# Performance work log

Hardware: AMD Instinct MI355X
Metric: run time of the kernel (lower is better)

The kernel has to match this reference:

```python
import jax, jax.numpy as jnp
import numpy as np

DIM = 768
NUM_HEADS = 12
HEAD_DIM = DIM // NUM_HEADS
SCALE = HEAD_DIM ** -0.5
NEG = -9e15


def setup_inputs() -> dict:
    key = jax.random.key(0)
    ks = jax.random.split(key, 8)
    B, N, M, C = 4, 1024, 2048, DIM
    q = jax.random.normal(ks[0], (B, N, C), dtype=jnp.float32)
    kv = jax.random.normal(ks[1], (B, M, C), dtype=jnp.float32)
    mask = jax.random.randint(ks[2], (B, 1, N, M), 0, 2, dtype=jnp.int32)
    s = 1.0 / np.sqrt(C)
    Wq = jax.random.normal(ks[3], (C, C), dtype=jnp.float32) * s      # nn.Linear(dim, dim), no bias
    Wkv = jax.random.normal(ks[4], (2 * C, C), dtype=jnp.float32) * s  # nn.Linear(dim, 2*dim), no bias
    Wproj = jax.random.normal(ks[5], (C, C), dtype=jnp.float32) * s
    bproj = jax.random.normal(ks[6], (C,), dtype=jnp.float32) * s
    return {"q": q, "kv": kv, "Wq": Wq, "Wkv": Wkv, "Wproj": Wproj, "bproj": bproj, "mask": mask}


def reference(q, kv, Wq, Wkv, Wproj, bproj, mask):
    B, M, C = kv.shape
    _, N, _ = q.shape
    H, d = NUM_HEADS, HEAD_DIM
    # kv projection -> [B, M, 2, H, d] -> k, v: [B, H, M, d]
    kvp = (kv @ Wkv.T).reshape(B, M, 2, H, d)
    k = kvp[:, :, 0].transpose(0, 2, 1, 3)
    v = kvp[:, :, 1].transpose(0, 2, 1, 3)
    # q projection -> [B, H, N, d], pre-scaled
    qp = (q @ Wq.T).reshape(B, N, H, d).transpose(0, 2, 1, 3) * SCALE
    attn = jnp.einsum('bhnd,bhmd->bhnm', qp, k)  # [B, H, N, M]
    attn = jnp.where(mask == 0, NEG, attn)
    attn = jax.nn.softmax(attn, axis=-1)
    # attn_drop / proj_drop have rate 0.0 (eval): identity
    x = jnp.einsum('bhnm,bhmd->bhnd', attn, v)
    x = x.transpose(0, 2, 1, 3).reshape(B, N, C)
    x = x @ Wproj.T + bproj
    return x
```

## Files before the change

### kernel.cpp

```cpp
#include <hip/hip_runtime.h>
#include <hip/hip_bf16.h>


typedef short    s16x8  __attribute__((ext_vector_type(8)));
typedef short    s16x4  __attribute__((ext_vector_type(4)));
typedef float    f32x4  __attribute__((ext_vector_type(4)));
typedef _Float16 f16x8  __attribute__((ext_vector_type(8)));
typedef _Float16 f16x4  __attribute__((ext_vector_type(4)));
typedef _Float16 f16x2  __attribute__((ext_vector_type(2)));

#define NUM_H 12
#define DIM   768
#define NQ    1024
#define MK    2048
#define QK_SCALE_LOG2E 0.18033688f

__device__ __forceinline__ short f2h(float v) {
    _Float16 h = (_Float16)v;
    return __builtin_bit_cast(short, h);
}
__device__ __forceinline__ f32x4 mfma16x32(f16x8 a, f16x8 b, f32x4 c) {
    return __builtin_amdgcn_mfma_f32_16x16x32_f16(a, b, c, 0, 0, 0);
}
__device__ __forceinline__ f16x2 pk2h(float a, float b) {
    return __builtin_bit_cast(f16x2, __builtin_amdgcn_cvt_pkrtz(a, b));
}
__device__ __forceinline__ void gl_lds16(const short* g, short* l) {
    __builtin_amdgcn_global_load_lds(
        (const __attribute__((address_space(1))) unsigned int*)g,
        (__attribute__((address_space(3))) unsigned int*)l, 16, 0, 0);
}

__global__ __launch_bounds__(256) void prep_kernel(
    const float* __restrict__ q, const float* __restrict__ kv,
    const float* __restrict__ Wq, const float* __restrict__ Wkv,
    const float* __restrict__ Wp, const int* __restrict__ mask,
    short* __restrict__ q_h, short* __restrict__ kv_h,
    short* __restrict__ Wq_h, short* __restrict__ Wkv_h,
    short* __restrict__ Wp_h, unsigned char* __restrict__ mbytes)
{
    int bid = blockIdx.x;
    if (bid < 5760) {
        const float* s; short* d; long base;
        if (bid < 1536)      { s = q;   d = q_h;   base = (long)bid * 2048; }
        else if (bid < 4608) { s = kv;  d = kv_h;  base = (long)(bid - 1536) * 2048; }
        else if (bid < 4896) { s = Wq;  d = Wq_h;  base = (long)(bid - 4608) * 2048; }
        else if (bid < 5472) { s = Wkv; d = Wkv_h; base = (long)(bid - 4896) * 2048; }
        else                 { s = Wp;  d = Wp_h;  base = (long)(bid - 5472) * 2048; }
        long i = base + threadIdx.x * 8;
        float4 a = *(const float4*)(s + i);
        float4 b = *(const float4*)(s + i + 4);
        s16x8 r;
        r[0] = f2h(a.x); r[1] = f2h(a.y); r[2] = f2h(a.z); r[3] = f2h(a.w);
        r[4] = f2h(b.x); r[5] = f2h(b.y); r[6] = f2h(b.z); r[7] = f2h(b.w);
        *(s16x8*)(d + i) = r;
    } else {
        long base = (long)(bid - 5760) * 2048 + threadIdx.x * 8;
        int4 m0 = *(const int4*)(mask + base);
        int4 m1 = *(const int4*)(mask + base + 4);
        unsigned v = (unsigned)(m0.x != 0)        | ((unsigned)(m0.y != 0) << 1)
                   | ((unsigned)(m0.z != 0) << 2) | ((unsigned)(m0.w != 0) << 3)
                   | ((unsigned)(m1.x != 0) << 4) | ((unsigned)(m1.y != 0) << 5)
                   | ((unsigned)(m1.z != 0) << 6) | ((unsigned)(m1.w != 0) << 7);
        mbytes[base >> 3] = (unsigned char)v;
    }
}

__device__ __forceinline__ void gemm_core(
    short* smem,
    const short* __restrict__ A, const short* __restrict__ Bt,
    int Ncols, int mode, const float* __restrict__ bias,
    short* __restrict__ outb, short* __restrict__ outb2,
    float* __restrict__ outf, int bid)
{
    short (*As)[64] = (short(*)[64])smem;
    short (*Bs)[64] = (short(*)[64])(smem + 8192);

    int ntiles = Ncols >> 7;
    int m0 = (bid / ntiles) << 7;
    int n0 = (bid % ntiles) << 7;
    int t = threadIdx.x;
    int w = t >> 6, lane = t & 63, quad = lane >> 4, l16 = lane & 15;
    int wm = (w & 1) << 6, wn = (w >> 1) << 6;

    f32x4 zero4 = {0.f, 0.f, 0.f, 0.f};
    f32x4 acc[4][4];
    for (int i = 0; i < 4; i++)
        for (int j = 0; j < 4; j++) acc[i][j] = zero4;

    const short* Ag = A + (long)(m0 + (w << 5) + (lane >> 3)) * DIM + ((lane & 7) << 3);
    const short* Bg = Bt + (long)(n0 + (w << 5) + (lane >> 3)) * DIM + ((lane & 7) << 3);
    short* Al = &As[w << 5][0];
    short* Bl = &Bs[w << 5][0];

    for (int kt = 0; kt < DIM; kt += 64) {
        __syncthreads();
        #pragma unroll
        for (int i = 0; i < 4; i++) {
            gl_lds16(Ag + (long)i * 8 * DIM + kt, Al + i * 512);
            gl_lds16(Bg + (long)i * 8 * DIM + kt, Bl + i * 512);
        }
        __syncthreads();
        #pragma unroll
        for (int kh = 0; kh < 2; kh++) {
            f16x8 af[4], bfr[4];
            #pragma unroll
            for (int i = 0; i < 4; i++)
                af[i] = __builtin_bit_cast(f16x8,
                    *(const s16x8*)&As[wm + i * 16 + l16][kh * 32 + quad * 8]);
            #pragma unroll
            for (int j = 0; j < 4; j++)
                bfr[j] = __builtin_bit_cast(f16x8,
                    *(const s16x8*)&Bs[wn + j * 16 + l16][kh * 32 + quad * 8]);
            #pragma unroll
            for (int i = 0; i < 4; i++)
                #pragma unroll
                for (int j = 0; j < 4; j++)
                    acc[i][j] = mfma16x32(af[i], bfr[j], acc[i][j]);
        }
    }

    __syncthreads();

    if (mode == 2) {
        #pragma unroll
        for (int i = 0; i < 4; i++)
            #pragma unroll
            for (int j = 0; j < 4; j++)
                #pragma unroll
                for (int r = 0; r < 4; r++) {
                    int row = m0 + wm + i * 16 + quad * 4 + r;
                    int col = n0 + wn + j * 16 + l16;
                    outf[(long)row * DIM + col] = acc[i][j][r] + bias[col];
                }
        return;
    }

    short (*Cs)[136] = (short(*)[136])smem;
    bool vreg = (mode == 1) && (n0 >= DIM);

    if (!vreg) {
        float sc = (mode == 0) ? QK_SCALE_LOG2E : 1.0f;
        #pragma unroll
        for (int i = 0; i < 4; i++)
            #pragma unroll
            for (int j = 0; j < 4; j++)
                #pragma unroll
                for (int r = 0; r < 4; r++)
                    Cs[wm + i * 16 + quad * 4 + r][wn + j * 16 + l16] =
                        f2h(acc[i][j][r] * sc);
    } else {
        #pragma unroll
        for (int i = 0; i < 4; i++)
            #pragma unroll
            for (int j = 0; j < 4; j++) {
                int c = wn + j * 16 + l16;
                int r0 = wm + i * 16 + quad * 4;
                s16x4 pk;
                pk[0] = f2h(acc[i][j][0]); pk[1] = f2h(acc[i][j][1]);
                pk[2] = f2h(acc[i][j][2]); pk[3] = f2h(acc[i][j][3]);
                *(s16x4*)&Cs[c][r0] = pk;
            }
    }
    __syncthreads();

    if (!vreg) {
        int hb2 = n0 >> 6;
        long rowsN = (mode == 0) ? NQ : MK;
        int b = (int)(m0 / rowsN);
        int rb = (int)(m0 % rowsN);
        short* ob0 = outb + ((long)(b * NUM_H + hb2) * rowsN + rb) * 64;
        short* ob1 = outb + ((long)(b * NUM_H + hb2 + 1) * rowsN + rb) * 64;
        #pragma unroll
        for (int k2 = 0; k2 < 8; k2++) {
            int ch = k2 * 256 + t;
            int half = ch >> 10, off = ch & 1023;
            s16x8 vd = *(const s16x8*)&Cs[off >> 3][(half << 6) + ((off & 7) << 3)];
            *(s16x8*)((half ? ob1 : ob0) + off * 8) = vd;
        }
    } else {
        int hb2 = (n0 - DIM) >> 6;
        int b = m0 >> 11, rb = m0 & 2047;
        #pragma unroll
        for (int k2 = 0; k2 < 8; k2++) {
            int ch = k2 * 256 + t;
            int c = ch >> 4, woff = (ch & 15) << 3;
            s16x8 vd = *(const s16x8*)&Cs[c][woff];
            int half = c >> 6, dd = c & 63;
            *(s16x8*)(outb2 + (((long)(b * NUM_H + hb2 + half) * 64 + dd) * MK + rb) + woff) = vd;
        }
    }
}

__global__ __launch_bounds__(256) void gemm12_kernel(
    const short* __restrict__ qh, const short* __restrict__ Wqh,
    const short* __restrict__ kvh, const short* __restrict__ Wkvh,
    short* __restrict__ qp, short* __restrict__ kk, short* __restrict__ vt)
{
    __shared__ short smem[18432];
    if (blockIdx.x < 192)
        gemm_core(smem, qh, Wqh, 768, 0, nullptr, qp, nullptr, nullptr, blockIdx.x);
    else
        gemm_core(smem, kvh, Wkvh, 1536, 1, nullptr, kk, vt, nullptr, blockIdx.x - 192);
}

__global__ __launch_bounds__(256) void gemm3_kernel(
    const short* __restrict__ xb, const short* __restrict__ Wph,
    const float* __restrict__ bias, float* __restrict__ out)
{
    __shared__ short smem[18432];
    gemm_core(smem, xb, Wph, 768, 2, bias, nullptr, nullptr, out, blockIdx.x);
}

__global__ __launch_bounds__(256) void attn_kernel(
    const short* __restrict__ qp, const short* __restrict__ kk,
    const short* __restrict__ vt, const unsigned* __restrict__ mb,
    short* __restrict__ xb)
{
    __shared__ short qs[64][72];
    __shared__ short ks[64][72];
    __shared__ short vs[64][72];

    int bid = blockIdx.x;
    int bh = bid % 48;
    int nt = bid / 48;
    int h = bh % NUM_H, b = bh / NUM_H;
    int n0 = nt << 6;
    int t = threadIdx.x, w = t >> 6, lane = t & 63, quad = lane >> 4, l16 = lane & 15;

    const short* qbase = qp + ((long)bh * NQ + n0) * 64;
    const short* kbase = kk + (long)bh * MK * 64;
    const short* vbase = vt + (long)bh * 64 * MK;
    const unsigned* mrow = mb + ((long)b * NQ + n0 + (w << 4) + l16) * 64;

    {
        int qr = t >> 2, c0 = (t & 3) << 4;
        *(s16x8*)&qs[qr][c0]     = *(const s16x8*)(qbase + qr * 64 + c0);
        *(s16x8*)&qs[qr][c0 + 8] = *(const s16x8*)(qbase + qr * 64 + c0 + 8);
    }
    __syncthreads();
    f16x8 bq[2];
    #pragma unroll
    for (int kh = 0; kh < 2; kh++)
        bq[kh] = __builtin_bit_cast(f16x8,
            *(const s16x8*)&qs[(w << 4) + l16][kh * 32 + quad * 8]);

    int sr = t >> 2, c0 = (t & 3) << 4;
    int pr = (sr & 32) + ((sr & 4) << 2) + ((sr & 24) >> 1) + (sr & 3);
    const short* kp = kbase + (long)sr * 64 + c0;
    const short* vp = vbase + (long)sr * MK + c0;

    s16x8 k0 = *(const s16x8*)(kp);
    s16x8 k1 = *(const s16x8*)(kp + 8);
    s16x8 v0 = *(const s16x8*)(vp);
    s16x8 v1 = *(const s16x8*)(vp + 8);
    uint2 mwv = *(const uint2*)(mrow);

    f32x4 zero4 = {0.f, 0.f, 0.f, 0.f};
    f32x4 o[4], ol = zero4;
    for (int j = 0; j < 4; j++) o[j] = zero4;
    const f16x8 ones = {(_Float16)1.f, (_Float16)1.f, (_Float16)1.f, (_Float16)1.f,
                        (_Float16)1.f, (_Float16)1.f, (_Float16)1.f, (_Float16)1.f};

    for (int mt = 0; mt < MK; mt += 64) {
        __syncthreads();
        *(s16x8*)&ks[pr][c0]     = k0;
        *(s16x8*)&ks[pr][c0 + 8] = k1;
        *(s16x8*)&vs[sr][c0]     = v0;
        *(s16x8*)&vs[sr][c0 + 8] = v1;
        unsigned cm0 = mwv.x, cm1 = mwv.y;
        __syncthreads();
        if (mt + 64 < MK) {
            k0 = *(const s16x8*)(kp + (long)(mt + 64) * 64);
            k1 = *(const s16x8*)(kp + (long)(mt + 64) * 64 + 8);
            v0 = *(const s16x8*)(vp + mt + 64);
            v1 = *(const s16x8*)(vp + mt + 64 + 8);
            mwv = *(const uint2*)(mrow + ((mt + 64) >> 5));
        }

        f32x4 s[4];
        #pragma unroll
        for (int jj = 0; jj < 4; jj++) s[jj] = zero4;
        #pragma unroll
        for (int kh = 0; kh < 2; kh++)
            #pragma unroll
            for (int jj = 0; jj < 4; jj++) {
                f16x8 ak = __builtin_bit_cast(f16x8,
                    *(const s16x8*)&ks[jj * 16 + l16][kh * 32 + quad * 8]);
                s[jj] = mfma16x32(ak, bq[kh], s[jj]);
            }

        f16x8 pa[2];
        #pragma unroll
        for (int j2 = 0; j2 < 2; j2++) {
            unsigned wsel = j2 ? cm1 : cm0;
            f16x2 pk[4];
            #pragma unroll
            for (int sub = 0; sub < 2; sub++) {
                unsigned bits = wsel >> ((quad << 3) + (sub << 2));
                const f32x4& sv = s[j2 * 2 + sub];
                float p0 = (bits & 1u)        ? __builtin_amdgcn_exp2f(sv[0]) : 0.f;
                float p1 = ((bits >> 1) & 1u) ? __builtin_amdgcn_exp2f(sv[1]) : 0.f;
                float p2 = ((bits >> 2) & 1u) ? __builtin_amdgcn_exp2f(sv[2]) : 0.f;
                float p3 = ((bits >> 3) & 1u) ? __builtin_amdgcn_exp2f(sv[3]) : 0.f;
                pk[sub * 2]     = pk2h(p0, p1);
                pk[sub * 2 + 1] = pk2h(p2, p3);
            }
            f16x4 lo = __builtin_shufflevector(pk[0], pk[1], 0, 1, 2, 3);
            f16x4 hi = __builtin_shufflevector(pk[2], pk[3], 0, 1, 2, 3);
            pa[j2] = __builtin_shufflevector(lo, hi, 0, 1, 2, 3, 4, 5, 6, 7);
        }

        #pragma unroll
        for (int j2 = 0; j2 < 2; j2++) {
            ol = mfma16x32(pa[j2], ones, ol);
            #pragma unroll
            for (int jd = 0; jd < 4; jd++) {
                f16x8 bv = __builtin_bit_cast(f16x8,
                    *(const s16x8*)&vs[jd * 16 + l16][j2 * 32 + quad * 8]);
                o[jd] = mfma16x32(pa[j2], bv, o[jd]);
            }
        }
    }

    float linv[4];
    #pragma unroll
    for (int rr = 0; rr < 4; rr++) linv[rr] = 1.0f / ol[rr];
    short (*ps)[72] = (short(*)[72])&qs[w << 4];
    #pragma unroll
    for (int jd = 0; jd < 4; jd++)
        #pragma unroll
        for (int rr = 0; rr < 4; rr++)
            ps[quad * 4 + rr][jd * 16 + l16] = f2h(o[jd][rr] * linv[rr]);

    #pragma unroll
    for (int k2 = 0; k2 < 2; k2++) {
        int row = (lane >> 3) + k2 * 8;
        int cc = (lane & 7) << 3;
        s16x8 vd = *(const s16x8*)&ps[row][cc];
        *(s16x8*)(xb + ((long)b * NQ + n0 + (w << 4) + row) * DIM + h * 64 + cc) = vd;
    }
}

extern "C" void kernel_launch(void* const* d_in, const int* in_sizes, int n_in,
                              void* d_out, int out_size, void* d_ws, size_t ws_size,
                              hipStream_t stream)
{
    const float* q     = (const float*)d_in[0];
    const float* kv    = (const float*)d_in[1];
    const float* Wq    = (const float*)d_in[2];
    const float* Wkv   = (const float*)d_in[3];
    const float* Wproj = (const float*)d_in[4];
    const float* bproj = (const float*)d_in[5];
    const int*   mask  = (const int*)d_in[6];
    float* out = (float*)d_out;

    char* ws = (char*)d_ws;
    short* q_h   = (short*)ws; ws += (size_t)4096 * 768 * 2;
    short* kv_h  = (short*)ws; ws += (size_t)8192 * 768 * 2;
    short* Wq_h  = (short*)ws; ws += (size_t)768 * 768 * 2;
    short* Wkv_h = (short*)ws; ws += (size_t)1536 * 768 * 2;
    short* Wp_h  = (short*)ws; ws += (size_t)768 * 768 * 2;
    short* qp    = (short*)ws; ws += (size_t)4096 * 768 * 2;
    short* kk    = (short*)ws; ws += (size_t)8192 * 768 * 2;
    short* vt    = (short*)ws; ws += (size_t)8192 * 768 * 2;
    short* xb    = (short*)ws; ws += (size_t)4096 * 768 * 2;
    unsigned char* mbytes = (unsigned char*)ws;

    prep_kernel<<<9856, 256, 0, stream>>>(q, kv, Wq, Wkv, Wproj, mask,
                                          q_h, kv_h, Wq_h, Wkv_h, Wp_h, mbytes);
    gemm12_kernel<<<960, 256, 0, stream>>>(q_h, Wq_h, kv_h, Wkv_h, qp, kk, vt);
    attn_kernel<<<768, 256, 0, stream>>>(qp, kk, vt, (const unsigned*)mbytes, xb);
    gemm3_kernel<<<192, 256, 0, stream>>>(xb, Wp_h, bproj, out);
}
```

Measured before the change: 221.4 us.

## Move mask packing into GEMM kernel and reorder tile rasterization

Mask bit-packing blocks move from the prep kernel into the projection GEMM launch as extra trailing blocks. The intent is to overlap the memory-bound mask read with compute-bound GEMM tiles, filling idle CUs during the GEMM tail. GEMM tile indexing also changes from row-major to column-major (M fastest), so concurrently running blocks share the same weight tile, which may improve L2 reuse of B. Launching many light blocks after the GEMM blocks could contend for bandwidth with the GEMM.

```diff
diff --git a/kernel.cpp b/kernel.cpp
--- a/kernel.cpp
+++ b/kernel.cpp
@@ -34,51 +34,39 @@
 __global__ __launch_bounds__(256) void prep_kernel(
     const float* __restrict__ q, const float* __restrict__ kv,
     const float* __restrict__ Wq, const float* __restrict__ Wkv,
-    const float* __restrict__ Wp, const int* __restrict__ mask,
+    const float* __restrict__ Wp,
     short* __restrict__ q_h, short* __restrict__ kv_h,
     short* __restrict__ Wq_h, short* __restrict__ Wkv_h,
-    short* __restrict__ Wp_h, unsigned char* __restrict__ mbytes)
+    short* __restrict__ Wp_h)
 {
     int bid = blockIdx.x;
-    if (bid < 5760) {
-        const float* s; short* d; long base;
-        if (bid < 1536)      { s = q;   d = q_h;   base = (long)bid * 2048; }
-        else if (bid < 4608) { s = kv;  d = kv_h;  base = (long)(bid - 1536) * 2048; }
-        else if (bid < 4896) { s = Wq;  d = Wq_h;  base = (long)(bid - 4608) * 2048; }
-        else if (bid < 5472) { s = Wkv; d = Wkv_h; base = (long)(bid - 4896) * 2048; }
-        else                 { s = Wp;  d = Wp_h;  base = (long)(bid - 5472) * 2048; }
-        long i = base + threadIdx.x * 8;
-        float4 a = *(const float4*)(s + i);
-        float4 b = *(const float4*)(s + i + 4);
-        s16x8 r;
-        r[0] = f2h(a.x); r[1] = f2h(a.y); r[2] = f2h(a.z); r[3] = f2h(a.w);
-        r[4] = f2h(b.x); r[5] = f2h(b.y); r[6] = f2h(b.z); r[7] = f2h(b.w);
-        *(s16x8*)(d + i) = r;
-    } else {
-        long base = (long)(bid - 5760) * 2048 + threadIdx.x * 8;
-        int4 m0 = *(const int4*)(mask + base);
-        int4 m1 = *(const int4*)(mask + base + 4);
-        unsigned v = (unsigned)(m0.x != 0)        | ((unsigned)(m0.y != 0) << 1)
-                   | ((unsigned)(m0.z != 0) << 2) | ((unsigned)(m0.w != 0) << 3)
-                   | ((unsigned)(m1.x != 0) << 4) | ((unsigned)(m1.y != 0) << 5)
-                   | ((unsigned)(m1.z != 0) << 6) | ((unsigned)(m1.w != 0) << 7);
-        mbytes[base >> 3] = (unsigned char)v;
-    }
+    const float* s; short* d; long base;
+    if (bid < 1536)      { s = q;   d = q_h;   base = (long)bid * 2048; }
+    else if (bid < 4608) { s = kv;  d = kv_h;  base = (long)(bid - 1536) * 2048; }
+    else if (bid < 4896) { s = Wq;  d = Wq_h;  base = (long)(bid - 4608) * 2048; }
+    else if (bid < 5472) { s = Wkv; d = Wkv_h; base = (long)(bid - 4896) * 2048; }
+    else                 { s = Wp;  d = Wp_h;  base = (long)(bid - 5472) * 2048; }
+    long i = base + threadIdx.x * 8;
+    float4 a = *(const float4*)(s + i);
+    float4 b = *(const float4*)(s + i + 4);
+    s16x8 r;
+    r[0] = f2h(a.x); r[1] = f2h(a.y); r[2] = f2h(a.z); r[3] = f2h(a.w);
+    r[4] = f2h(b.x); r[5] = f2h(b.y); r[6] = f2h(b.z); r[7] = f2h(b.w);
+    *(s16x8*)(d + i) = r;
 }
 
 __device__ __forceinline__ void gemm_core(
     short* smem,
     const short* __restrict__ A, const short* __restrict__ Bt,
-    int Ncols, int mode, const float* __restrict__ bias,
+    int mtiles, int mode, const float* __restrict__ bias,
     short* __restrict__ outb, short* __restrict__ outb2,
     float* __restrict__ outf, int bid)
 {
     short (*As)[64] = (short(*)[64])smem;
     short (*Bs)[64] = (short(*)[64])(smem + 8192);
 
-    int ntiles = Ncols >> 7;
-    int m0 = (bid / ntiles) << 7;
-    int n0 = (bid % ntiles) << 7;
+    int m0 = (bid % mtiles) << 7;
+    int n0 = (bid / mtiles) << 7;
     int t = threadIdx.x;
     int w = t >> 6, lane = t & 63, quad = lane >> 4, l16 = lane & 15;
     int wm = (w & 1) << 6, wn = (w >> 1) << 6;
@@ -195,13 +183,26 @@
 __global__ __launch_bounds__(256) void gemm12_kernel(
     const short* __restrict__ qh, const short* __restrict__ Wqh,
     const short* __restrict__ kvh, const short* __restrict__ Wkvh,
-    short* __restrict__ qp, short* __restrict__ kk, short* __restrict__ vt)
+    short* __restrict__ qp, short* __restrict__ kk, short* __restrict__ vt,
+    const int* __restrict__ mask, unsigned char* __restrict__ mbytes)
 {
     __shared__ short smem[18432];
-    if (blockIdx.x < 192)
-        gemm_core(smem, qh, Wqh, 768, 0, nullptr, qp, nullptr, nullptr, blockIdx.x);
+    int bid = blockIdx.x;
+    if (bid >= 960) {
+        long base = (long)(bid - 960) * 2048 + threadIdx.x * 8;
+        int4 m0 = *(const int4*)(mask + base);
+        int4 m1 = *(const int4*)(mask + base + 4);
+        unsigned v = (unsigned)(m0.x != 0)        | ((unsigned)(m0.y != 0) << 1)
+                   | ((unsigned)(m0.z != 0) << 2) | ((unsigned)(m0.w != 0) << 3)
+                   | ((unsigned)(m1.x != 0) << 4) | ((unsigned)(m1.y != 0) << 5)
+                   | ((unsigned)(m1.z != 0) << 6) | ((unsigned)(m1.w != 0) << 7);
+        mbytes[base >> 3] = (unsigned char)v;
+        return;
+    }
+    if (bid < 192)
+        gemm_core(smem, qh, Wqh, 32, 0, nullptr, qp, nullptr, nullptr, bid);
     else
-        gemm_core(smem, kvh, Wkvh, 1536, 1, nullptr, kk, vt, nullptr, blockIdx.x - 192);
+        gemm_core(smem, kvh, Wkvh, 64, 1, nullptr, kk, vt, nullptr, bid - 192);
 }
 
 __global__ __launch_bounds__(256) void gemm3_kernel(
@@ -209,7 +210,7 @@
     const float* __restrict__ bias, float* __restrict__ out)
 {
     __shared__ short smem[18432];
-    gemm_core(smem, xb, Wph, 768, 2, bias, nullptr, nullptr, out, blockIdx.x);
+    gemm_core(smem, xb, Wph, 32, 2, bias, nullptr, nullptr, out, blockIdx.x);
 }
 
 __global__ __launch_bounds__(256) void attn_kernel(
@@ -367,9 +368,10 @@
     short* xb    = (short*)ws; ws += (size_t)4096 * 768 * 2;
     unsigned char* mbytes = (unsigned char*)ws;
 
-    prep_kernel<<<9856, 256, 0, stream>>>(q, kv, Wq, Wkv, Wproj, mask,
-                                          q_h, kv_h, Wq_h, Wkv_h, Wp_h, mbytes);
-    gemm12_kernel<<<960, 256, 0, stream>>>(q_h, Wq_h, kv_h, Wkv_h, qp, kk, vt);
+    prep_kernel<<<5760, 256, 0, stream>>>(q, kv, Wq, Wkv, Wproj,
+                                          q_h, kv_h, Wq_h, Wkv_h, Wp_h);
+    gemm12_kernel<<<5056, 256, 0, stream>>>(q_h, Wq_h, kv_h, Wkv_h,
+                                            qp, kk, vt, mask, mbytes);
     attn_kernel<<<768, 256, 0, stream>>>(qp, kk, vt, (const unsigned*)mbytes, xb);
     gemm3_kernel<<<192, 256, 0, stream>>>(xb, Wp_h, bproj, out);
 }
```

New measurement: 222.0 us. No clear change (+0.3%).
